# Optimization experiments

Measured on AMD Instinct MI355X. Metric: run time of the kernel, lower is better.

## Reference

```python
import jax, jax.numpy as jnp
import numpy as np

L, C, FC, H, W, K = 6, 256, 1024, 4, 10, 3
B, T = 4, 1024
KC = C // H


def _get_rel_emb(emb, length):
    # emb: [1, 2W+1, KC] -> [1, 2*length-1, KC]
    pad_len = max(length - (W + 1), 0)
    start = max(W + 1 - length, 0)
    if pad_len > 0:
        emb = jnp.pad(emb, ((0, 0), (pad_len, pad_len), (0, 0)))
    return emb[:, start:start + 2 * length - 1]


def _rel_to_abs(x):
    # [b,h,l,2l-1] -> [b,h,l,l] via pad/reshape shift trick
    b, h, l, _ = x.shape
    x = jnp.pad(x, ((0, 0), (0, 0), (0, 0), (0, 1)))
    x = x.reshape(b, h, l * 2 * l)
    x = jnp.pad(x, ((0, 0), (0, 0), (0, l - 1)))
    return x.reshape(b, h, l + 1, 2 * l - 1)[:, :, :l, l - 1:]


def _abs_to_rel(x):
    # [b,h,l,l] -> [b,h,l,2l-1]
    b, h, l, _ = x.shape
    x = jnp.pad(x, ((0, 0), (0, 0), (0, 0), (0, l - 1)))
    x = x.reshape(b, h, l * l + l * (l - 1))
    x = jnp.pad(x, ((0, 0), (0, 0), (l, 0)))
    return x.reshape(b, h, l, 2 * l)[:, :, :, 1:]


def _ln(x, g, b, eps=1e-5):
    # channel-wise LayerNorm over dim 1 of [B,C,T]
    m = x.mean(axis=1, keepdims=True)
    v = ((x - m) ** 2).mean(axis=1, keepdims=True)
    return (x - m) * jax.lax.rsqrt(v + eps) * g[None, :, None] + b[None, :, None]


def _conv1(x, w, b):
    # pointwise Conv1d: x [B,Cin,T], w [Cout,Cin]
    return jnp.einsum('oc,bct->bot', w, x) + b[None, :, None]


def _convk(x, w, b):
    # Conv1d: x [B,Cin,Tpad], w [Cout,Cin,K], VALID
    y = jax.lax.conv_general_dilated(x, w, (1,), 'VALID', dimension_numbers=('NCH', 'OIH', 'NCH'))
    return y + b[None, :, None]


def _attn(x, mask, wq, bq, wk, bk, wv, bv, wo, bo, erk, erv):
    b, d, t = x.shape
    q = _conv1(x, wq, bq)
    k = _conv1(x, wk, bk)
    v = _conv1(x, wv, bv)
    def split(z):
        return z.reshape(b, H, KC, t).transpose(0, 1, 3, 2)  # [b,h,t,kc]
    qh = split(q) / np.sqrt(KC).astype(np.float32)
    kh = split(k)
    vh = split(v)
    scores = jnp.einsum('bhld,bhmd->bhlm', qh, kh)
    rel_k = _get_rel_emb(erk, t)[0]  # [2t-1, kc]
    scores = scores + _rel_to_abs(jnp.einsum('bhld,md->bhlm', qh, rel_k))
    scores = jnp.where(mask == 0, jnp.float32(-1e4), scores)
    p = jax.nn.softmax(scores, axis=-1)
    out = jnp.einsum('bhlm,bhmd->bhld', p, vh)
    rel_v = _get_rel_emb(erv, t)[0]
    out = out + jnp.einsum('bhlm,md->bhld', _abs_to_rel(p), rel_v)
    out = out.transpose(0, 1, 3, 2).reshape(b, d, t)
    return _conv1(out, wo, bo)


def _ffn(x, mask, w1, b1, w2, b2):
    pl, pr = (K - 1) // 2, K // 2
    def pad_t(z):
        return jnp.pad(z * mask, ((0, 0), (0, 0), (pl, pr)))
    h = jax.nn.relu(_convk(pad_t(x), w1, b1))
    return _convk(pad_t(h), w2, b2) * mask


def setup_inputs() -> dict:
    key = jax.random.key(0)
    ks = jax.random.split(key, 12)
    s = 0.05
    return {
        'x': jax.random.normal(ks[0], (B, C, T), jnp.float32),
        'x_mask': jnp.ones((B, 1, T), jnp.float32),
        'wq': s * jax.random.normal(ks[1], (L, C, C), jnp.float32),
        'bq': jnp.zeros((L, C), jnp.float32),
        'wk': s * jax.random.normal(ks[2], (L, C, C), jnp.float32),
        'bk': jnp.zeros((L, C), jnp.float32),
        'wv': s * jax.random.normal(ks[3], (L, C, C), jnp.float32),
        'bv': jnp.zeros((L, C), jnp.float32),
        'wo': s * jax.random.normal(ks[4], (L, C, C), jnp.float32),
        'bo': jnp.zeros((L, C), jnp.float32),
        'erk': (KC ** -0.5) * jax.random.normal(ks[5], (L, 1, 2 * W + 1, KC), jnp.float32),
        'erv': (KC ** -0.5) * jax.random.normal(ks[6], (L, 1, 2 * W + 1, KC), jnp.float32),
        'ln1_g': jnp.ones((L, C), jnp.float32),
        'ln1_b': jnp.zeros((L, C), jnp.float32),
        'ffn_w1': s * jax.random.normal(ks[7], (L, FC, C, K), jnp.float32),
        'ffn_b1': jnp.zeros((L, FC), jnp.float32),
        'ffn_w2': s * jax.random.normal(ks[8], (L, C, FC, K), jnp.float32),
        'ffn_b2': jnp.zeros((L, C), jnp.float32),
        'ln2_g': jnp.ones((L, C), jnp.float32),
        'ln2_b': jnp.zeros((L, C), jnp.float32),
    }


def reference(x, x_mask, wq, bq, wk, bk, wv, bv, wo, bo, erk, erv, ln1_g, ln1_b, ffn_w1, ffn_b1, ffn_w2, ffn_b2, ln2_g, ln2_b):
    attn_mask = x_mask[:, :, None, :] * x_mask[:, :, :, None]  # [B,1,T,T]
    x = x * x_mask
    for i in range(L):
        y = _attn(x, attn_mask, wq[i], bq[i], wk[i], bk[i], wv[i], bv[i], wo[i], bo[i], erk[i], erv[i])
        x = _ln(x + y, ln1_g[i], ln1_b[i])
        y = _ffn(x, x_mask, ffn_w1[i], ffn_b1[i], ffn_w2[i], ffn_b2[i])
        x = _ln(x + y, ln2_g[i], ln2_b[i])
    return x * x_mask
```

## Files before the change

### kernel.cpp

```cpp
#include <hip/hip_runtime.h>


#define Lz 6
#define Cz 256
#define FCz 1024
#define Hz 4
#define Wz 10
#define Bz 4
#define Tz 1024
#define KCz 64
#define NR 21
#define TS 1032
#define PADF 4
#define PROWS 1026
#define MFIX 8.0f

typedef unsigned short u16;
typedef unsigned int u32;
typedef __attribute__((ext_vector_type(8))) short bf8v;
typedef __attribute__((ext_vector_type(4))) float f4v;

#define MFMA(a, b, c) __builtin_amdgcn_mfma_f32_16x16x32_bf16(a, b, c, 0, 0, 0)

__device__ inline void bf_split(float v, u16& hi, u16& lo) {
  unsigned u = __float_as_uint(v);
  unsigned hr = (u + 0x7FFFu + ((u >> 16) & 1u)) >> 16;
  float rem = v - __uint_as_float(hr << 16);
  unsigned u2 = __float_as_uint(rem);
  unsigned lr = (u2 + 0x7FFFu + ((u2 >> 16) & 1u)) >> 16;
  hi = (u16)hr;
  lo = (u16)lr;
}

__device__ inline u16 bf_rne(float v) {
  u32 u = __float_as_uint(v);
  return (u16)((u + 0x7FFFu + ((u >> 16) & 1u)) >> 16);
}

__global__ __launch_bounds__(256) void mask_in(const float* __restrict__ x,
                                               const float* __restrict__ m,
                                               float* __restrict__ xp) {
  int id = blockIdx.x * 256 + threadIdx.x;
  if (id < Bz * Cz * Tz) {
    int t = id & (Tz - 1), row = id >> 10, b = id >> 18;
    xp[(size_t)row * TS + PADF + t] = x[id] * m[b * Tz + t];
  }
}

__global__ __launch_bounds__(256) void mask_out(const float* __restrict__ xp,
                                                const float* __restrict__ m,
                                                float* __restrict__ out) {
  int id = blockIdx.x * 256 + threadIdx.x;
  if (id < Bz * Cz * Tz) {
    int t = id & (Tz - 1), row = id >> 10, b = id >> 18;
    out[id] = xp[(size_t)row * TS + PADF + t] * m[b * Tz + t];
  }
}

__global__ __launch_bounds__(256) void zero_halo(u16* hi, u16* lo, int Cd) {
  int id = blockIdx.x * 256 + threadIdx.x;
  if (id >= Bz * 2 * Cd) return;
  int c = id % Cd, rb = id / Cd, b = rb >> 1, s = rb & 1;
  size_t a = ((size_t)b * PROWS + (s ? (PROWS - 1) : 0)) * Cd + c;
  hi[a] = 0;
  lo[a] = 0;
}

__global__ __launch_bounds__(256) void tpack(const float* __restrict__ src,
                                             const float* __restrict__ mask,
                                             u16* __restrict__ dhi,
                                             u16* __restrict__ dlo, int Cd) {
  __shared__ float L[64 * 68];
  const int tid = threadIdx.x;
  const int t0 = blockIdx.x * 64, c0 = blockIdx.y * 64, b = blockIdx.z;
  const float* sb = src + (size_t)b * Cd * TS + PADF;
#pragma unroll
  for (int i = 0; i < 16; i++) {
    int id = tid + 256 * i;
    int cc = id >> 6, tt = id & 63;
    L[cc * 68 + tt] = sb[(size_t)(c0 + cc) * TS + t0 + tt];
  }
  __syncthreads();
  const int tt = tid >> 2, p = tid & 3;
  float mv = mask[(size_t)b * Tz + t0 + tt];
  u16 hs[16], ls[16];
#pragma unroll
  for (int j = 0; j < 16; j++) {
    float v = L[(p * 16 + j) * 68 + tt] * mv;
    bf_split(v, hs[j], ls[j]);
  }
  size_t da = ((size_t)b * PROWS + t0 + tt + 1) * Cd + c0 + p * 16;
  *(uint4*)&dhi[da] = *(uint4*)&hs[0];
  *(uint4*)&dhi[da + 8] = *(uint4*)&hs[8];
  *(uint4*)&dlo[da] = *(uint4*)&ls[0];
  *(uint4*)&dlo[da + 8] = *(uint4*)&ls[8];
}

__global__ __launch_bounds__(256) void pack_all(
    const float* __restrict__ wq, const float* __restrict__ wk,
    const float* __restrict__ wv, const float* __restrict__ wo_,
    const float* __restrict__ bq, const float* __restrict__ bk,
    const float* __restrict__ bv, const float* __restrict__ bo,
    const float* __restrict__ erk, const float* __restrict__ erv,
    const float* __restrict__ fw1, const float* __restrict__ fw2,
    u16* __restrict__ qwAll, float* __restrict__ pbAll,
    u16* __restrict__ ekAll, u16* __restrict__ evAll,
    u16* __restrict__ w1All, u16* __restrict__ w2All) {
  const int blk = blockIdx.x, tid = threadIdx.x;
  const int layer = blk / 7184;
  const int bl = blk % 7184;
  if (bl < 1024) {
    int id = bl * 256 + tid;
    int o = id >> 8, c = id & 255;
    int sel = o >> 8;
    const size_t wof = (size_t)layer * Cz * Cz;
    const float* w = sel == 0 ? wq + wof
                              : (sel == 1 ? wk + wof
                                          : (sel == 2 ? wv + wof : wo_ + wof));
    qwAll[(size_t)layer * 262144 + id] = bf_rne(w[((o & 255) << 8) + c]);
    if (id < 1024) {
      int s2 = id >> 8;
      const float* bs = s2 == 0 ? bq : (s2 == 1 ? bk : (s2 == 2 ? bv : bo));
      pbAll[layer * 1024 + id] = bs[layer * Cz + (id & 255)];
    }
  } else if (bl < 1040) {
    int id = (bl - 1024) * 256 + tid;
    if (id < 2048) {
      int rr = id >> 6, d = id & 63;
      ekAll[layer * 2048 + id] =
          bf_rne((rr < NR) ? erk[(size_t)layer * NR * KCz + rr * KCz + d]
                           : 0.f);
    } else {
      int id2 = id - 2048;
      int d = id2 >> 5, rr = id2 & 31;
      evAll[layer * 2048 + id2] =
          bf_rne((rr < NR) ? erv[(size_t)layer * NR * KCz + rr * KCz + d]
                           : 0.f);
    }
  } else if (bl < 4112) {
    int id = (bl - 1040) * 256 + tid;
    int c = id % Cz;
    int rest = id / Cz;
    int o = rest % FCz, tap = rest / FCz;
    w1All[(size_t)layer * 786432 + id] =
        bf_rne(fw1[(size_t)layer * FCz * Cz * 3 + ((size_t)o * Cz + c) * 3 +
                   tap]);
  } else {
    int id = (bl - 4112) * 256 + tid;
    int c = id % FCz;
    int rest = id / FCz;
    int o = rest % Cz, tap = rest / Cz;
    w2All[(size_t)layer * 786432 + id] =
        bf_rne(fw2[(size_t)layer * Cz * FCz * 3 + ((size_t)o * FCz + c) * 3 +
                   tap]);
  }
}

template <int EPI>
__global__ __launch_bounds__(256) void mfma_gemm2(
    const u16* __restrict__ Ah, const u16* __restrict__ Bh,
    const u16* __restrict__ Bl, const float* __restrict__ bias,
    const float* __restrict__ mask, float* __restrict__ out,
    float* __restrict__ out2, u16* __restrict__ pqh, u16* __restrict__ pql,
    u16* __restrict__ pkh, u16* __restrict__ pvh, int M, int Kc, int m_base) {
  __shared__ __align__(16) char smraw[17408];
  u16* Ash = (u16*)smraw;
  u16* Bsh = Ash + 2560;
  u16* Bsl = Bsh + 2560;
  const int tid = threadIdx.x;
  const int lane = tid & 63, wid = tid >> 6;
  const int wm = wid & 1, wn = wid >> 1;
  const int r = lane & 15, qd = lane >> 4;
  const int t0 = blockIdx.x * 64;
  const int b = blockIdx.z;
  const int srow = tid >> 2, sseg = (tid & 3) * 8;

  int m0, kc0, kcN;
  float* outp = out;
  if constexpr (EPI == 3) {
    m0 = m_base + (blockIdx.y >> 1) * 64;
    kc0 = (blockIdx.y & 1) * (Kc / 2);
    kcN = Kc / 2;
    outp = (blockIdx.y & 1) ? out2 : out;
  } else {
    m0 = blockIdx.y * 64 + m_base;
    kc0 = 0;
    kcN = Kc;
  }

  f4v acc[2][2];
#pragma unroll
  for (int i = 0; i < 2; i++)
#pragma unroll
    for (int j = 0; j < 2; j++) acc[i][j] = (f4v)(0.f);

  const size_t arow = (size_t)(m0 + srow) * Kc + kc0;
  const size_t brow = ((size_t)b * PROWS + t0 + 1 + srow) * Kc + kc0;
  for (int kc = 0; kc < kcN; kc += 32) {
    *(uint4*)&Ash[srow * 40 + sseg] = *(const uint4*)&Ah[arow + kc + sseg];
    *(uint4*)&Bsh[srow * 40 + sseg] = *(const uint4*)&Bh[brow + kc + sseg];
    *(uint4*)&Bsl[srow * 40 + sseg] = *(const uint4*)&Bl[brow + kc + sseg];
    __syncthreads();
    bf8v ah[2], bh2[2], bl2[2];
#pragma unroll
    for (int f = 0; f < 2; f++) {
      int ar = (wm * 32 + f * 16 + r) * 40 + qd * 8;
      int br = (wn * 32 + f * 16 + r) * 40 + qd * 8;
      ah[f] = *(bf8v*)&Ash[ar];
      bh2[f] = *(bf8v*)&Bsh[br];
      bl2[f] = *(bf8v*)&Bsl[br];
    }
#pragma unroll
    for (int mf = 0; mf < 2; mf++)
#pragma unroll
      for (int nf = 0; nf < 2; nf++) {
        acc[mf][nf] = MFMA(ah[mf], bh2[nf], acc[mf][nf]);
        acc[mf][nf] = MFMA(ah[mf], bl2[nf], acc[mf][nf]);
      }
    __syncthreads();
  }

  float* Ds = (float*)smraw;
  if constexpr (EPI == 0) {
    const int sel = m0 >> 8;
    const int h = (m0 >> 6) & 3;
    const int bhI = b * Hz + h;
    if (sel < 2) {
#pragma unroll
      for (int mf = 0; mf < 2; mf++)
#pragma unroll
        for (int nf = 0; nf < 2; nf++) {
          int nl = wn * 32 + nf * 16 + r;
          int ml = wm * 32 + mf * 16 + qd * 4;
          *(f4v*)&Ds[nl * 68 + ml] = acc[mf][nf];
        }
      __syncthreads();
      const int row = tid >> 2, p = tid & 3;
      size_t da = ((size_t)bhI * Tz + t0 + row) * KCz + p * 16;
      if (sel == 0) {
        u16 hs[16], ls[16];
#pragma unroll
        for (int jj = 0; jj < 4; jj++) {
          float4 dv = *(float4*)&Ds[row * 68 + p * 16 + jj * 4];
          float4 bb = *(const float4*)&bias[m0 + p * 16 + jj * 4];
          float vv[4] = {(dv.x + bb.x) * 0.125f, (dv.y + bb.y) * 0.125f,
                         (dv.z + bb.z) * 0.125f, (dv.w + bb.w) * 0.125f};
#pragma unroll
          for (int e = 0; e < 4; e++)
            bf_split(vv[e], hs[jj * 4 + e], ls[jj * 4 + e]);
        }
        *(uint4*)&pqh[da] = *(uint4*)&hs[0];
        *(uint4*)&pqh[da + 8] = *(uint4*)&hs[8];
        *(uint4*)&pql[da] = *(uint4*)&ls[0];
        *(uint4*)&pql[da + 8] = *(uint4*)&ls[8];
      } else {
        u16 hs[16];
#pragma unroll
        for (int jj = 0; jj < 4; jj++) {
          float4 dv = *(float4*)&Ds[row * 68 + p * 16 + jj * 4];
          float4 bb = *(const float4*)&bias[m0 + p * 16 + jj * 4];
          hs[jj * 4 + 0] = bf_rne(dv.x + bb.x);
          hs[jj * 4 + 1] = bf_rne(dv.y + bb.y);
          hs[jj * 4 + 2] = bf_rne(dv.z + bb.z);
          hs[jj * 4 + 3] = bf_rne(dv.w + bb.w);
        }
        *(uint4*)&pkh[da] = *(uint4*)&hs[0];
        *(uint4*)&pkh[da + 8] = *(uint4*)&hs[8];
      }
    } else {
#pragma unroll
      for (int mf = 0; mf < 2; mf++)
#pragma unroll
        for (int nf = 0; nf < 2; nf++) {
          int ml = wm * 32 + mf * 16 + qd * 4;
          int nl = wn * 32 + nf * 16 + r;
#pragma unroll
          for (int e = 0; e < 4; e++) Ds[(ml + e) * 68 + nl] = acc[mf][nf][e];
        }
      __syncthreads();
      const int row = tid >> 2, p = tid & 3;
      const float bb = bias[m0 + row];
      u16 hs[16];
#pragma unroll
      for (int jj = 0; jj < 16; jj++)
        hs[jj] = bf_rne(Ds[row * 68 + p * 16 + jj] + bb);
      size_t da = ((size_t)bhI * KCz + row) * Tz + t0 + p * 16;
      *(uint4*)&pvh[da] = *(uint4*)&hs[0];
      *(uint4*)&pvh[da + 8] = *(uint4*)&hs[8];
    }
  } else {
#pragma unroll
    for (int mf = 0; mf < 2; mf++)
#pragma unroll
      for (int nf = 0; nf < 2; nf++) {
        int ml = wm * 32 + mf * 16 + qd * 4;
        int nl = wn * 32 + nf * 16 + r;
#pragma unroll
        for (int e = 0; e < 4; e++) Ds[(ml + e) * 68 + nl] = acc[mf][nf][e];
      }
    __syncthreads();
    const int row = tid >> 2, p = tid & 3;
    size_t oa = ((size_t)b * Cz + (m0 - m_base) + row) * Tz + t0 + p * 16;
#pragma unroll
    for (int jj = 0; jj < 4; jj++)
      *(float4*)&outp[oa + jj * 4] = *(float4*)&Ds[row * 68 + p * 16 + jj * 4];
  }
}

template <int EPI>
__global__ __launch_bounds__(256) void conv_mfma(
    const u16* __restrict__ Ah, const u16* __restrict__ Bh,
    const u16* __restrict__ Bl, const float* __restrict__ bias,
    const float* __restrict__ mask, u16* __restrict__ ph,
    u16* __restrict__ pl, float* __restrict__ o0, float* __restrict__ o1,
    float* __restrict__ o2, float* __restrict__ o3, int M, int Kc) {
  __shared__ __align__(16) char smraw[34816];
  u16* Ash = (u16*)smraw;
  u16* Bsh = Ash + 2560;
  u16* Bsl = Bsh + 5120;
  const int tid = threadIdx.x;
  const int lane = tid & 63, wid = tid >> 6;
  const int wm = wid & 1, wn = wid >> 1;
  const int r = lane & 15, qd = lane >> 4;
  const int t0 = blockIdx.x * 128;
  const int b = blockIdx.z;
  const int sarow = tid >> 2, saseg = (tid & 3) * 8;
  const int sbrow = tid >> 1, sbseg = (tid & 1) * 16;

  int m0, kc0, kcN;
  float* outp = nullptr;
  if constexpr (EPI == 3) {
    int mt = blockIdx.y >> 2, sp = blockIdx.y & 3;
    m0 = mt * 64;
    kc0 = sp * (Kc / 4);
    kcN = Kc / 4;
    outp = sp == 0 ? o0 : (sp == 1 ? o1 : (sp == 2 ? o2 : o3));
  } else {
    m0 = blockIdx.y * 64;
    kc0 = 0;
    kcN = Kc;
  }

  f4v acc[2][4];
#pragma unroll
  for (int i = 0; i < 2; i++)
#pragma unroll
    for (int j = 0; j < 4; j++) acc[i][j] = (f4v)(0.f);

  for (int tap = 0; tap < 3; tap++) {
    const u16* At = Ah + (size_t)tap * M * Kc;
    const size_t arow = (size_t)(m0 + sarow) * Kc + kc0;
    const size_t brow = ((size_t)b * PROWS + t0 + tap + sbrow) * Kc + kc0;
    for (int kc = 0; kc < kcN; kc += 32) {
      *(uint4*)&Ash[sarow * 40 + saseg] = *(const uint4*)&At[arow + kc + saseg];
      *(uint4*)&Bsh[sbrow * 40 + sbseg] = *(const uint4*)&Bh[brow + kc + sbseg];
      *(uint4*)&Bsh[sbrow * 40 + sbseg + 8] =
          *(const uint4*)&Bh[brow + kc + sbseg + 8];
      *(uint4*)&Bsl[sbrow * 40 + sbseg] = *(const uint4*)&Bl[brow + kc + sbseg];
      *(uint4*)&Bsl[sbrow * 40 + sbseg + 8] =
          *(const uint4*)&Bl[brow + kc + sbseg + 8];
      __syncthreads();
      bf8v ah[2], bh4[4], bl4[4];
#pragma unroll
      for (int mf = 0; mf < 2; mf++)
        ah[mf] = *(bf8v*)&Ash[(wm * 32 + mf * 16 + r) * 40 + qd * 8];
#pragma unroll
      for (int nf = 0; nf < 4; nf++) {
        int br = (wn * 64 + nf * 16 + r) * 40 + qd * 8;
        bh4[nf] = *(bf8v*)&Bsh[br];
        bl4[nf] = *(bf8v*)&Bsl[br];
      }
#pragma unroll
      for (int mf = 0; mf < 2; mf++)
#pragma unroll
        for (int nf = 0; nf < 4; nf++) {
          acc[mf][nf] = MFMA(ah[mf], bh4[nf], acc[mf][nf]);
          acc[mf][nf] = MFMA(ah[mf], bl4[nf], acc[mf][nf]);
        }
      __syncthreads();
    }
  }

  if constexpr (EPI == 1) {
    float* Ds = (float*)smraw;
#pragma unroll
    for (int mf = 0; mf < 2; mf++)
#pragma unroll
      for (int nf = 0; nf < 4; nf++) {
        int nl = wn * 64 + nf * 16 + r;
        int ml = wm * 32 + mf * 16 + qd * 4;
        *(f4v*)&Ds[nl * 68 + ml] = acc[mf][nf];
      }
    __syncthreads();
    const int row = tid >> 1, half = (tid & 1) * 32;
    const int t = t0 + row;
    const float mv = mask[(size_t)b * Tz + t];
    u16 hs[32], ls[32];
#pragma unroll
    for (int j = 0; j < 32; j += 4) {
      float4 dv = *(float4*)&Ds[row * 68 + half + j];
      float4 bb = *(const float4*)&bias[m0 + half + j];
      float vv[4] = {dv.x + bb.x, dv.y + bb.y, dv.z + bb.z, dv.w + bb.w};
#pragma unroll
      for (int e = 0; e < 4; e++) {
        float v = fmaxf(vv[e], 0.f) * mv;
        bf_split(v, hs[j + e], ls[j + e]);
      }
    }
    size_t da = ((size_t)b * PROWS + t + 1) * M + m0 + half;
#pragma unroll
    for (int j = 0; j < 32; j += 8) {
      *(uint4*)&ph[da + j] = *(uint4*)&hs[j];
      *(uint4*)&pl[da + j] = *(uint4*)&ls[j];
    }
  } else {
    float* Ds = (float*)smraw;
#pragma unroll
    for (int mf = 0; mf < 2; mf++)
#pragma unroll
      for (int nf = 0; nf < 4; nf++) {
        int ml = wm * 32 + mf * 16 + qd * 4;
        int nl = wn * 64 + nf * 16 + r;
#pragma unroll
        for (int e = 0; e < 4; e++) Ds[(ml + e) * 132 + nl] = acc[mf][nf][e];
      }
    __syncthreads();
    const int row = tid >> 2, seg = (tid & 3) * 32;
    size_t oa = ((size_t)b * Cz + m0 + row) * Tz + t0 + seg;
#pragma unroll
    for (int j = 0; j < 8; j++)
      *(float4*)&outp[oa + j * 4] = *(float4*)&Ds[row * 132 + seg + j * 4];
  }
}

__global__ __launch_bounds__(128, 2) void attn_mfma(
    const u16* __restrict__ Qh_, const u16* __restrict__ Ql_,
    const u16* __restrict__ Kh_, const u16* __restrict__ Vh_,
    const float* __restrict__ mask, const u16* __restrict__ erkH,
    const u16* __restrict__ ervH, float* __restrict__ O0,
    float* __restrict__ O1, float* __restrict__ O2, float* __restrict__ O3,
    float* __restrict__ lp0, float* __restrict__ lp1,
    float* __restrict__ lp2, float* __restrict__ lp3) {
  __shared__ __align__(16) char smraw[2][14336];
  const int tid = threadIdx.x;
  const int lane = tid & 63, wid = tid >> 6;
  const int r = lane & 15, qd = lane >> 4;
  const int idx = blockIdx.x;
  const int bh = idx & 15;
  const int split = (idx >> 4) & 3;
  const int i0w = (idx >> 6) * 64 + wid * 32;
  const int b = bh >> 2, h = bh & 3;
  const float* mb = mask + (size_t)b * Tz;
  const size_t qkbase = (size_t)bh * Tz * KCz;
  const size_t vbase = (size_t)bh * KCz * Tz;
  float* Op = split == 0 ? O0 : (split == 1 ? O1 : (split == 2 ? O2 : O3));
  float* lp = split == 0 ? lp0 : (split == 1 ? lp1 : (split == 2 ? lp2 : lp3));
  const int j0beg = split * 256;

  float* rqs = (float*)(smraw[wid]);
  float* bands = rqs + 704;
  u16* Pp = (u16*)(smraw[wid] + 5632);

  bf8v qh[2][2], ql[2][2];
#pragma unroll
  for (int rs = 0; rs < 2; rs++) {
    const size_t qrow = qkbase + (size_t)(i0w + rs * 16 + r) * KCz;
#pragma unroll
    for (int ks = 0; ks < 2; ks++) {
      qh[rs][ks] = *(const bf8v*)&Qh_[qrow + ks * 32 + qd * 8];
      ql[rs][ks] = *(const bf8v*)&Ql_[qrow + ks * 32 + qd * 8];
    }
  }
  for (int t = lane; t < 704; t += 64) bands[t] = -1e30f;

#pragma unroll
  for (int rs = 0; rs < 2; rs++) {
    f4v rc[2] = {(f4v)(0.f), (f4v)(0.f)};
#pragma unroll
    for (int nf = 0; nf < 2; nf++)
#pragma unroll
      for (int ks = 0; ks < 2; ks++) {
        bf8v eh = *(const bf8v*)&erkH[(16 * nf + r) * 64 + ks * 32 + qd * 8];
        rc[nf] = MFMA(qh[rs][ks], eh, rc[nf]);
        rc[nf] = MFMA(ql[rs][ks], eh, rc[nf]);
      }
#pragma unroll
    for (int nf = 0; nf < 2; nf++) {
      int rr = 16 * nf + r;
      if (rr < NR) {
#pragma unroll
        for (int e = 0; e < 4; e++)
          rqs[(rs * 16 + 4 * qd + e) * 22 + rr] = rc[nf][e];
      }
    }
  }

  float qm[2][4];
#pragma unroll
  for (int rs = 0; rs < 2; rs++)
#pragma unroll
    for (int e = 0; e < 4; e++) qm[rs][e] = mb[i0w + rs * 16 + 4 * qd + e];

  float lacc[2][4] = {};
  f4v oacc[2][4];
#pragma unroll
  for (int rs = 0; rs < 2; rs++)
#pragma unroll
    for (int nf = 0; nf < 4; nf++) oacc[rs][nf] = (f4v)(0.f);

#pragma unroll 2
  for (int jt = 0; jt < 4; jt++) {
    const int j0 = j0beg + jt * 64;
    bf8v kh[4][2], vh[4][2];
#pragma unroll
    for (int nf = 0; nf < 4; nf++) {
      const size_t kr = qkbase + (size_t)(j0 + 16 * nf + r) * KCz;
      const size_t vr = vbase + (size_t)(16 * nf + r) * Tz + j0;
#pragma unroll
      for (int ks = 0; ks < 2; ks++) {
        kh[nf][ks] = *(const bf8v*)&Kh_[kr + ks * 32 + qd * 8];
        vh[nf][ks] = *(const bf8v*)&Vh_[vr + ks * 32 + qd * 8];
      }
    }
    float km4[4];
#pragma unroll
    for (int nf = 0; nf < 4; nf++) km4[nf] = mb[j0 + 16 * nf + r];

#pragma unroll
    for (int rs = 0; rs < 2; rs++) {
      f4v sa[4];
#pragma unroll
      for (int nf = 0; nf < 4; nf++) sa[nf] = (f4v)(0.f);
#pragma unroll
      for (int nf = 0; nf < 4; nf++)
#pragma unroll
        for (int ks = 0; ks < 2; ks++) {
          sa[nf] = MFMA(qh[rs][ks], kh[nf][ks], sa[nf]);
          sa[nf] = MFMA(ql[rs][ks], kh[nf][ks], sa[nf]);
        }
      const int ibase = i0w + rs * 16;
      const bool diag = (j0 + 63 >= ibase - Wz) && (j0 <= ibase + 15 + Wz);
#pragma unroll
      for (int nf = 0; nf < 4; nf++)
#pragma unroll
        for (int e = 0; e < 4; e++) {
          const int iloc = rs * 16 + 4 * qd + e;
          float s = sa[nf][e];
          if (diag) {
            int dl = (j0 + 16 * nf + r) - (i0w + iloc);
            bool inb = (unsigned)(dl + Wz) <= 2u * Wz;
            if (inb) s += rqs[iloc * 22 + dl + Wz];
            if (qm[rs][e] * km4[nf] == 0.f) s = -1e4f;
            if (inb) bands[iloc * 22 + dl + Wz] = s;
          } else {
            if (qm[rs][e] * km4[nf] == 0.f) s = -1e4f;
          }
          float p = __expf(s - MFIX);
          lacc[rs][e] += p;
          Pp[iloc * 72 + 16 * nf + r] = bf_rne(p);
        }
    }
#pragma unroll
    for (int rs = 0; rs < 2; rs++)
#pragma unroll
      for (int ks = 0; ks < 2; ks++) {
        bf8v Ph = *(bf8v*)&Pp[(rs * 16 + r) * 72 + ks * 32 + qd * 8];
#pragma unroll
        for (int nf = 0; nf < 4; nf++)
          oacc[rs][nf] = MFMA(Ph, vh[nf][ks], oacc[rs][nf]);
      }
  }

  for (int t = lane; t < 32 * 32; t += 64) {
    int i = t >> 5, rr = t & 31;
    float p = (rr < NR) ? __expf(bands[i * 22 + rr] - MFIX) : 0.f;
    Pp[i * 72 + rr] = bf_rne(p);
  }
#pragma unroll
  for (int rs = 0; rs < 2; rs++) {
    bf8v Ph = *(bf8v*)&Pp[(rs * 16 + r) * 72 + qd * 8];
#pragma unroll
    for (int nf = 0; nf < 4; nf++) {
      bf8v eh = *(const bf8v*)&ervH[(16 * nf + r) * 32 + qd * 8];
      oacc[rs][nf] = MFMA(Ph, eh, oacc[rs][nf]);
    }
  }

#pragma unroll
  for (int off = 1; off < 16; off <<= 1)
#pragma unroll
    for (int rs = 0; rs < 2; rs++)
#pragma unroll
      for (int e = 0; e < 4; e++)
        lacc[rs][e] += __shfl_xor(lacc[rs][e], off, 16);
  if (r == 0) {
#pragma unroll
    for (int rs = 0; rs < 2; rs++)
#pragma unroll
      for (int e = 0; e < 4; e++)
        lp[(size_t)bh * Tz + i0w + rs * 16 + 4 * qd + e] = lacc[rs][e];
  }

  float* Os = (float*)Pp;
#pragma unroll
  for (int rs = 0; rs < 2; rs++)
#pragma unroll
    for (int nf = 0; nf < 4; nf++)
#pragma unroll
      for (int e = 0; e < 4; e++)
        Os[(rs * 16 + 4 * qd + e) * 68 + 16 * nf + r] = oacc[rs][nf][e];
#pragma unroll
  for (int rs = 0; rs < 2; rs++) {
    const float* src = &Os[(rs * 16 + r) * 68 + qd * 16];
    size_t oa = ((size_t)bh * Tz + i0w + rs * 16 + r) * KCz + qd * 16;
#pragma unroll
    for (int jj = 0; jj < 4; jj++)
      *(float4*)&Op[oa + jj * 4] = *(const float4*)&src[jj * 4];
  }
}

__global__ __launch_bounds__(256) void attn_combine(
    const float* __restrict__ O0, const float* __restrict__ O1,
    const float* __restrict__ O2, const float* __restrict__ O3,
    const float* __restrict__ l0, const float* __restrict__ l1,
    const float* __restrict__ l2, const float* __restrict__ l3,
    u16* __restrict__ outH, u16* __restrict__ outL) {
  const int bh = blockIdx.y, b = bh >> 2, h = bh & 3;
  const int i = blockIdx.x * 16 + (threadIdx.x >> 4);
  const int d0 = (threadIdx.x & 15) * 4;
  const size_t oa = ((size_t)bh * Tz + i) * KCz + d0;
  float4 a = *(const float4*)&O0[oa];
  float4 c = *(const float4*)&O1[oa];
  float4 d = *(const float4*)&O2[oa];
  float4 f = *(const float4*)&O3[oa];
  const size_t la = (size_t)bh * Tz + i;
  const float li = 1.f / (l0[la] + l1[la] + l2[la] + l3[la]);
  float v[4] = {(a.x + c.x + d.x + f.x) * li, (a.y + c.y + d.y + f.y) * li,
                (a.z + c.z + d.z + f.z) * li, (a.w + c.w + d.w + f.w) * li};
  u16 hs[4], ls[4];
#pragma unroll
  for (int e = 0; e < 4; e++) bf_split(v[e], hs[e], ls[e]);
  size_t da = ((size_t)b * PROWS + i + 1) * Cz + h * 64 + d0;
  *(uint2*)&outH[da] = *(uint2*)&hs[0];
  *(uint2*)&outL[da] = *(uint2*)&ls[0];
}

template <int VAR, int NP>
__global__ __launch_bounds__(256) void fused_ln(
    float* __restrict__ x, const float* __restrict__ y,
    const float* __restrict__ p1, const float* __restrict__ p2,
    const float* __restrict__ p3, const float* __restrict__ cbias,
    const float* __restrict__ g, const float* __restrict__ bb,
    const float* __restrict__ mask, u16* __restrict__ dhi,
    u16* __restrict__ dlo) {
  __shared__ float L[256 * 17];
  __shared__ float red[16][16], red2[16][16];
  __shared__ float ms[16], rs[16];
  const int tid = threadIdx.x;
  const int t0 = blockIdx.x * 16, b = blockIdx.y;
  const int tl = tid & 15, grp = tid >> 4;
  const size_t bx = (size_t)b * Cz * TS + PADF + t0 + tl;
  const size_t by = (size_t)b * Cz * Tz + t0 + tl;
  const float mv = mask[(size_t)b * Tz + t0 + tl];
  float s = 0.f, sq = 0.f;
  for (int c = grp; c < Cz; c += 16) {
    float add = y[by + (size_t)c * Tz] + p1[by + (size_t)c * Tz] + cbias[c];
    if constexpr (NP == 4)
      add += p2[by + (size_t)c * Tz] + p3[by + (size_t)c * Tz];
    if constexpr (VAR == 1) add *= mv;
    float v = x[bx + (size_t)c * TS] + add;
    L[c * 17 + tl] = v;
    s += v;
    sq += v * v;
  }
  red[grp][tl] = s;
  red2[grp][tl] = sq;
  __syncthreads();
  if (tid < 16) {
    float su = 0.f, sqq = 0.f;
#pragma unroll
    for (int gg = 0; gg < 16; gg++) {
      su += red[gg][tid];
      sqq += red2[gg][tid];
    }
    float m = su * (1.f / Cz);
    ms[tid] = m;
    rs[tid] = rsqrtf(sqq * (1.f / Cz) - m * m + 1e-5f);
  }
  __syncthreads();
  float m = ms[tl], r = rs[tl];
  for (int c = grp; c < Cz; c += 16) {
    float v = (L[c * 17 + tl] - m) * r * g[c] + bb[c];
    x[bx + (size_t)c * TS] = v;
    L[c * 17 + tl] = v * mv;
  }
  __syncthreads();
  const int tt = tid & 15, p = tid >> 4;
  u16 hs[16], ls[16];
#pragma unroll
  for (int j = 0; j < 16; j++)
    bf_split(L[(p * 16 + j) * 17 + tt], hs[j], ls[j]);
  size_t da = ((size_t)b * PROWS + t0 + tt + 1) * Cz + p * 16;
  *(uint4*)&dhi[da] = *(uint4*)&hs[0];
  *(uint4*)&dhi[da + 8] = *(uint4*)&hs[8];
  *(uint4*)&dlo[da] = *(uint4*)&ls[0];
  *(uint4*)&dlo[da + 8] = *(uint4*)&ls[8];
}

extern "C" void kernel_launch(void* const* d_in, const int* in_sizes, int n_in,
                              void* d_out, int out_size, void* d_ws,
                              size_t ws_size, hipStream_t stream) {
  const float* x = (const float*)d_in[0];
  const float* xm = (const float*)d_in[1];
  const float* wq = (const float*)d_in[2];
  const float* bq = (const float*)d_in[3];
  const float* wk = (const float*)d_in[4];
  const float* bk = (const float*)d_in[5];
  const float* wv = (const float*)d_in[6];
  const float* bv = (const float*)d_in[7];
  const float* wo = (const float*)d_in[8];
  const float* bo = (const float*)d_in[9];
  const float* erk = (const float*)d_in[10];
  const float* erv = (const float*)d_in[11];
  const float* g1 = (const float*)d_in[12];
  const float* b1 = (const float*)d_in[13];
  const float* fw1 = (const float*)d_in[14];
  const float* fb1 = (const float*)d_in[15];
  const float* fw2 = (const float*)d_in[16];
  const float* fb2 = (const float*)d_in[17];
  const float* g2 = (const float*)d_in[18];
  const float* b2 = (const float*)d_in[19];

  const size_t NBC = (size_t)Bz * Cz * Tz;
  const size_t XBN = (size_t)Bz * Cz * TS;
  const size_t HP = (size_t)Bz * PROWS * FCz;
  const size_t XP = (size_t)Bz * PROWS * Cz;
  const size_t QS = (size_t)Bz * Hz * Tz * KCz;

  float* ws = (float*)d_ws;
  float* xb = ws;
  float* yb = xb + XBN;
  float* p1 = yb + NBC;
  float* p2 = p1 + NBC;
  float* p3 = p2 + NBC;
  float* unf = p3 + NBC;
  u16* hpH = (u16*)unf;
  u16* hpL = hpH + HP;
  u16* Qh = (u16*)unf;
  u16* Ql = Qh + QS;
  u16* Kh = Ql + QS;
  u16* Vh = Kh + QS;
  float* xpf = unf + HP;
  u16* xpH = (u16*)xpf;
  u16* xpL = xpH + XP;
  float* qwf = xpf + XP;
  u16* qwAll = (u16*)qwf;
  float* w1f = qwf + 786432;
  u16* w1All = (u16*)w1f;
  float* w2f = w1f + 2359296;
  u16* w2All = (u16*)w2f;
  float* erf = w2f + 2359296;
  u16* ekAll = (u16*)erf;
  u16* evAll = ekAll + 12288;
  float* pbAll = erf + 12288;
  float* lb0 = pbAll + 6144;
  float* lb1 = lb0 + 16384;
  float* lb2 = lb1 + 16384;
  float* lb3 = lb2 + 16384;

  const int ntot = (int)NBC;
  pack_all<<<dim3(6 * 7184), 256, 0, stream>>>(
      wq, wk, wv, wo, bq, bk, bv, bo, erk, erv, fw1, fw2, qwAll, pbAll, ekAll,
      evAll, w1All, w2All);
  mask_in<<<dim3((ntot + 255) / 256), 256, 0, stream>>>(x, xm, xb);
  zero_halo<<<dim3((Bz * 2 * Cz + 255) / 256), 256, 0, stream>>>(xpH, xpL, Cz);
  tpack<<<dim3(16, 4, 4), 256, 0, stream>>>(xb, xm, xpH, xpL, Cz);

  for (int l = 0; l < Lz; l++) {
    mfma_gemm2<0><<<dim3(16, 12, 4), 256, 0, stream>>>(
        qwAll + (size_t)l * 262144, xpH, xpL, pbAll + l * 1024, xm, nullptr,
        nullptr, Qh, Ql, Kh, Vh, 1024, Cz, 0);
    attn_mfma<<<dim3(1024), 128, 0, stream>>>(
        Qh, Ql, Kh, Vh, xm, ekAll + l * 2048, evAll + l * 2048, yb, p1, p2, p3,
        lb0, lb1, lb2, lb3);
    attn_combine<<<dim3(64, 16), 256, 0, stream>>>(yb, p1, p2, p3, lb0, lb1,
                                                   lb2, lb3, xpH, xpL);
    mfma_gemm2<3><<<dim3(16, 8, 4), 256, 0, stream>>>(
        qwAll + (size_t)l * 262144, xpH, xpL, pbAll + l * 1024, xm, yb, p1,
        nullptr, nullptr, nullptr, nullptr, 1024, Cz, 768);
    fused_ln<2, 2><<<dim3(64, 4), 256, 0, stream>>>(
        xb, yb, p1, nullptr, nullptr, bo + l * Cz, g1 + l * Cz, b1 + l * Cz,
        xm, xpH, xpL);
    zero_halo<<<dim3((Bz * 2 * FCz + 255) / 256), 256, 0, stream>>>(hpH, hpL,
                                                                    FCz);
    conv_mfma<1><<<dim3(8, 16, 4), 256, 0, stream>>>(
        w1All + (size_t)l * 786432, xpH, xpL, fb1 + l * FCz, xm, hpH, hpL,
        nullptr, nullptr, nullptr, nullptr, FCz, Cz);
    conv_mfma<3><<<dim3(8, 16, 4), 256, 0, stream>>>(
        w2All + (size_t)l * 786432, hpH, hpL, nullptr, xm, nullptr, nullptr,
        yb, p1, p2, p3, Cz, FCz);
    fused_ln<1, 4><<<dim3(64, 4), 256, 0, stream>>>(
        xb, yb, p1, p2, p3, fb2 + l * Cz, g2 + l * Cz, b2 + l * Cz, xm, xpH,
        xpL);
  }
  mask_out<<<dim3((ntot + 255) / 256), 256, 0, stream>>>(xb, xm,
                                                         (float*)d_out);
}
```

Baseline: 1.005 ms.

## Enlarge FFN conv tiles to 128x128 with shared B window across taps and register prefetch

The FFN convolution kernel now uses 512 threads and a 128x128 output tile. It loads the B (activation) rows once per k-chunk as a 130-row window that all three taps reuse through a row offset, instead of reloading B for each tap. It also prefetches the next k-chunk's A and B into registers while the current chunk's MFMAs run. The grid halves, so there are fewer blocks (256 per conv) and more shared memory per block, which may lower occupancy. The epilogues are split into two half-tile passes to fit the staging buffer.

```diff
diff --git a/kernel.cpp b/kernel.cpp
--- a/kernel.cpp
+++ b/kernel.cpp
@@ -308,128 +308,161 @@
 }
 
 template <int EPI>
-__global__ __launch_bounds__(256) void conv_mfma(
+__global__ __launch_bounds__(512) void conv_mfma(
     const u16* __restrict__ Ah, const u16* __restrict__ Bh,
     const u16* __restrict__ Bl, const float* __restrict__ bias,
     const float* __restrict__ mask, u16* __restrict__ ph,
     u16* __restrict__ pl, float* __restrict__ o0, float* __restrict__ o1,
     float* __restrict__ o2, float* __restrict__ o3, int M, int Kc) {
-  __shared__ __align__(16) char smraw[34816];
+  __shared__ __align__(16) char smraw[51840];
   u16* Ash = (u16*)smraw;
-  u16* Bsh = Ash + 2560;
-  u16* Bsl = Bsh + 5120;
+  u16* Bsh = Ash + 3 * 128 * 40;
+  u16* Bsl = Bsh + 132 * 40;
   const int tid = threadIdx.x;
   const int lane = tid & 63, wid = tid >> 6;
   const int wm = wid & 1, wn = wid >> 1;
   const int r = lane & 15, qd = lane >> 4;
   const int t0 = blockIdx.x * 128;
   const int b = blockIdx.z;
-  const int sarow = tid >> 2, saseg = (tid & 3) * 8;
-  const int sbrow = tid >> 1, sbseg = (tid & 1) * 16;
 
   int m0, kc0, kcN;
   float* outp = nullptr;
   if constexpr (EPI == 3) {
     int mt = blockIdx.y >> 2, sp = blockIdx.y & 3;
-    m0 = mt * 64;
+    m0 = mt * 128;
     kc0 = sp * (Kc / 4);
     kcN = Kc / 4;
     outp = sp == 0 ? o0 : (sp == 1 ? o1 : (sp == 2 ? o2 : o3));
   } else {
-    m0 = blockIdx.y * 64;
+    m0 = blockIdx.y * 128;
     kc0 = 0;
     kcN = Kc;
   }
 
-  f4v acc[2][4];
-#pragma unroll
-  for (int i = 0; i < 2; i++)
-#pragma unroll
-    for (int j = 0; j < 4; j++) acc[i][j] = (f4v)(0.f);
-
-  for (int tap = 0; tap < 3; tap++) {
-    const u16* At = Ah + (size_t)tap * M * Kc;
-    const size_t arow = (size_t)(m0 + sarow) * Kc + kc0;
-    const size_t brow = ((size_t)b * PROWS + t0 + tap + sbrow) * Kc + kc0;
-    for (int kc = 0; kc < kcN; kc += 32) {
-      *(uint4*)&Ash[sarow * 40 + saseg] = *(const uint4*)&At[arow + kc + saseg];
-      *(uint4*)&Bsh[sbrow * 40 + sbseg] = *(const uint4*)&Bh[brow + kc + sbseg];
-      *(uint4*)&Bsh[sbrow * 40 + sbseg + 8] =
-          *(const uint4*)&Bh[brow + kc + sbseg + 8];
-      *(uint4*)&Bsl[sbrow * 40 + sbseg] = *(const uint4*)&Bl[brow + kc + sbseg];
-      *(uint4*)&Bsl[sbrow * 40 + sbseg + 8] =
-          *(const uint4*)&Bl[brow + kc + sbseg + 8];
+  const int srow = tid >> 2, sseg = (tid & 3) * 8;
+  const bool btail = tid < 8;
+  const int brow2 = 128 + (tid >> 2);
+
+  f4v acc[4][2];
+#pragma unroll
+  for (int i = 0; i < 4; i++)
+#pragma unroll
+    for (int j = 0; j < 2; j++) acc[i][j] = (f4v)(0.f);
+
+  const size_t abase = (size_t)(m0 + srow) * Kc + kc0 + sseg;
+  const size_t bbase = ((size_t)b * PROWS + t0 + srow) * Kc + kc0 + sseg;
+  const size_t bbase2 = ((size_t)b * PROWS + t0 + brow2) * Kc + kc0 + sseg;
+
+  uint4 ar[3], bhr, blr, bhr2, blr2;
+  auto LOADR = [&](int kc) {
+#pragma unroll
+    for (int tp = 0; tp < 3; tp++)
+      ar[tp] = *(const uint4*)&Ah[(size_t)tp * M * Kc + abase + kc];
+    bhr = *(const uint4*)&Bh[bbase + kc];
+    blr = *(const uint4*)&Bl[bbase + kc];
+    if (btail) {
+      bhr2 = *(const uint4*)&Bh[bbase2 + kc];
+      blr2 = *(const uint4*)&Bl[bbase2 + kc];
+    }
+  };
+
+  LOADR(0);
+  for (int kc = 0; kc < kcN; kc += 32) {
+#pragma unroll
+    for (int tp = 0; tp < 3; tp++)
+      *(uint4*)&Ash[(tp * 128 + srow) * 40 + sseg] = ar[tp];
+    *(uint4*)&Bsh[srow * 40 + sseg] = bhr;
+    *(uint4*)&Bsl[srow * 40 + sseg] = blr;
+    if (btail) {
+      *(uint4*)&Bsh[brow2 * 40 + sseg] = bhr2;
+      *(uint4*)&Bsl[brow2 * 40 + sseg] = blr2;
+    }
+    __syncthreads();
+    if (kc + 32 < kcN) LOADR(kc + 32);
+#pragma unroll
+    for (int tap = 0; tap < 3; tap++) {
+      bf8v ah[4], bh2[2], bl2[2];
+#pragma unroll
+      for (int mf = 0; mf < 4; mf++)
+        ah[mf] =
+            *(bf8v*)&Ash[(tap * 128 + wm * 64 + mf * 16 + r) * 40 + qd * 8];
+#pragma unroll
+      for (int nf = 0; nf < 2; nf++) {
+        int br = (wn * 32 + nf * 16 + r + tap) * 40 + qd * 8;
+        bh2[nf] = *(bf8v*)&Bsh[br];
+        bl2[nf] = *(bf8v*)&Bsl[br];
+      }
+#pragma unroll
+      for (int mf = 0; mf < 4; mf++)
+#pragma unroll
+        for (int nf = 0; nf < 2; nf++) {
+          acc[mf][nf] = MFMA(ah[mf], bh2[nf], acc[mf][nf]);
+          acc[mf][nf] = MFMA(ah[mf], bl2[nf], acc[mf][nf]);
+        }
+    }
+    __syncthreads();
+  }
+
+  float* Ds = (float*)smraw;
+  if constexpr (EPI == 1) {
+#pragma unroll
+    for (int h = 0; h < 2; h++) {
+      if ((wn >> 1) == h) {
+#pragma unroll
+        for (int mf = 0; mf < 4; mf++)
+#pragma unroll
+          for (int nf = 0; nf < 2; nf++) {
+            int tl = (wn & 1) * 32 + nf * 16 + r;
+            int ml = wm * 64 + mf * 16 + qd * 4;
+            *(f4v*)&Ds[tl * 132 + ml] = acc[mf][nf];
+          }
+      }
       __syncthreads();
-      bf8v ah[2], bh4[4], bl4[4];
-#pragma unroll
-      for (int mf = 0; mf < 2; mf++)
-        ah[mf] = *(bf8v*)&Ash[(wm * 32 + mf * 16 + r) * 40 + qd * 8];
-#pragma unroll
-      for (int nf = 0; nf < 4; nf++) {
-        int br = (wn * 64 + nf * 16 + r) * 40 + qd * 8;
-        bh4[nf] = *(bf8v*)&Bsh[br];
-        bl4[nf] = *(bf8v*)&Bsl[br];
-      }
-#pragma unroll
-      for (int mf = 0; mf < 2; mf++)
-#pragma unroll
-        for (int nf = 0; nf < 4; nf++) {
-          acc[mf][nf] = MFMA(ah[mf], bh4[nf], acc[mf][nf]);
-          acc[mf][nf] = MFMA(ah[mf], bl4[nf], acc[mf][nf]);
+      const int row = tid >> 3, mseg = (tid & 7) * 16;
+      const int t = t0 + h * 64 + row;
+      const float mv = mask[(size_t)b * Tz + t];
+      u16 hs[16], ls[16];
+#pragma unroll
+      for (int j = 0; j < 16; j += 4) {
+        float4 dv = *(float4*)&Ds[row * 132 + mseg + j];
+        float4 bb = *(const float4*)&bias[m0 + mseg + j];
+        float vv[4] = {dv.x + bb.x, dv.y + bb.y, dv.z + bb.z, dv.w + bb.w};
+#pragma unroll
+        for (int e = 0; e < 4; e++) {
+          float v = fmaxf(vv[e], 0.f) * mv;
+          bf_split(v, hs[j + e], ls[j + e]);
         }
+      }
+      size_t da = ((size_t)b * PROWS + t + 1) * M + m0 + mseg;
+      *(uint4*)&ph[da] = *(uint4*)&hs[0];
+      *(uint4*)&ph[da + 8] = *(uint4*)&hs[8];
+      *(uint4*)&pl[da] = *(uint4*)&ls[0];
+      *(uint4*)&pl[da + 8] = *(uint4*)&ls[8];
       __syncthreads();
     }
-  }
-
-  if constexpr (EPI == 1) {
-    float* Ds = (float*)smraw;
-#pragma unroll
-    for (int mf = 0; mf < 2; mf++)
-#pragma unroll
-      for (int nf = 0; nf < 4; nf++) {
-        int nl = wn * 64 + nf * 16 + r;
-        int ml = wm * 32 + mf * 16 + qd * 4;
-        *(f4v*)&Ds[nl * 68 + ml] = acc[mf][nf];
-      }
-    __syncthreads();
-    const int row = tid >> 1, half = (tid & 1) * 32;
-    const int t = t0 + row;
-    const float mv = mask[(size_t)b * Tz + t];
-    u16 hs[32], ls[32];
-#pragma unroll
-    for (int j = 0; j < 32; j += 4) {
-      float4 dv = *(float4*)&Ds[row * 68 + half + j];
-      float4 bb = *(const float4*)&bias[m0 + half + j];
-      float vv[4] = {dv.x + bb.x, dv.y + bb.y, dv.z + bb.z, dv.w + bb.w};
-#pragma unroll
-      for (int e = 0; e < 4; e++) {
-        float v = fmaxf(vv[e], 0.f) * mv;
-        bf_split(v, hs[j + e], ls[j + e]);
-      }
-    }
-    size_t da = ((size_t)b * PROWS + t + 1) * M + m0 + half;
-#pragma unroll
-    for (int j = 0; j < 32; j += 8) {
-      *(uint4*)&ph[da + j] = *(uint4*)&hs[j];
-      *(uint4*)&pl[da + j] = *(uint4*)&ls[j];
-    }
   } else {
-    float* Ds = (float*)smraw;
-#pragma unroll
-    for (int mf = 0; mf < 2; mf++)
-#pragma unroll
-      for (int nf = 0; nf < 4; nf++) {
-        int ml = wm * 32 + mf * 16 + qd * 4;
-        int nl = wn * 64 + nf * 16 + r;
-#pragma unroll
-        for (int e = 0; e < 4; e++) Ds[(ml + e) * 132 + nl] = acc[mf][nf][e];
-      }
-    __syncthreads();
-    const int row = tid >> 2, seg = (tid & 3) * 32;
-    size_t oa = ((size_t)b * Cz + m0 + row) * Tz + t0 + seg;
-#pragma unroll
-    for (int j = 0; j < 8; j++)
-      *(float4*)&outp[oa + j * 4] = *(float4*)&Ds[row * 132 + seg + j * 4];
+#pragma unroll
+    for (int h = 0; h < 2; h++) {
+      if (wm == h) {
+#pragma unroll
+        for (int mf = 0; mf < 4; mf++)
+#pragma unroll
+          for (int nf = 0; nf < 2; nf++) {
+            int ml = mf * 16 + qd * 4;
+            int nl = wn * 32 + nf * 16 + r;
+#pragma unroll
+            for (int e = 0; e < 4; e++)
+              Ds[(ml + e) * 132 + nl] = acc[mf][nf][e];
+          }
+      }
+      __syncthreads();
+      const int row = tid >> 3, tseg = (tid & 7) * 16;
+      size_t oa = ((size_t)b * Cz + m0 + h * 64 + row) * Tz + t0 + tseg;
+#pragma unroll
+      for (int j = 0; j < 4; j++)
+        *(float4*)&outp[oa + j * 4] = *(float4*)&Ds[row * 132 + tseg + j * 4];
+      __syncthreads();
+    }
   }
 }
 
@@ -793,10 +826,10 @@
         xm, xpH, xpL);
     zero_halo<<<dim3((Bz * 2 * FCz + 255) / 256), 256, 0, stream>>>(hpH, hpL,
                                                                     FCz);
-    conv_mfma<1><<<dim3(8, 16, 4), 256, 0, stream>>>(
+    conv_mfma<1><<<dim3(8, 8, 4), 512, 0, stream>>>(
         w1All + (size_t)l * 786432, xpH, xpL, fb1 + l * FCz, xm, hpH, hpL,
         nullptr, nullptr, nullptr, nullptr, FCz, Cz);
-    conv_mfma<3><<<dim3(8, 16, 4), 256, 0, stream>>>(
+    conv_mfma<3><<<dim3(8, 8, 4), 512, 0, stream>>>(
         w2All + (size_t)l * 786432, hpH, hpL, nullptr, xm, nullptr, nullptr,
         yb, p1, p2, p3, Cz, FCz);
     fused_ln<1, 4><<<dim3(64, 4), 256, 0, stream>>>(
```

New measurement: 1.035 ms. 1.03x slower.
